# Optimization experiments

Measured on AMD Instinct MI355X. Metric: run time of the kernel, lower is better.

The kernel has to match this reference:

```python
import jax, jax.numpy as jnp
import numpy as np

NUM_EXPERTS = 64
TOP_K = 2
HIDDEN = 4096
BATCH, SEQ = 4, 4096


def setup_inputs() -> dict:
    key = jax.random.key(0)
    k1, k2 = jax.random.split(key)
    hidden_states = jax.random.normal(k1, (BATCH, SEQ, HIDDEN), dtype=jnp.float32)
    # nn.init.normal_(gate.weight, std=0.02); Linear weight shape [E, H]
    gate_w = jax.random.normal(k2, (NUM_EXPERTS, HIDDEN), dtype=jnp.float32) * 0.02
    return {"hidden_states": hidden_states, "gate_w": gate_w}


def reference(hidden_states, gate_w):
    b, s, h = hidden_states.shape
    num_tokens = b * s
    hidden_flat = hidden_states.reshape(num_tokens, h)            # [N, H]
    router_logits = jnp.einsum('nh,eh->ne', hidden_flat, gate_w)  # [N, E]
    routing_probs = jax.nn.softmax(router_logits, axis=-1)        # [N, E]
    topk_probs, topk_indices = jax.lax.top_k(routing_probs, TOP_K)  # [N, K]
    # normalize_weights=True
    topk_probs = topk_probs / (topk_probs.sum(axis=-1, keepdims=True) + 1e-8)
    # routing index computation (grouped-GEMM dispatch metadata)
    flat_experts = topk_indices.reshape(-1)                        # [N*K]
    gather_indices = jnp.argsort(flat_experts, stable=True)        # token_indices[sort_order] == sort_order
    expert_counts = jnp.zeros((NUM_EXPERTS,), dtype=jnp.int32).at[flat_experts].add(1)
    expert_offsets = jnp.cumsum(expert_counts, axis=0)             # [E]
    routing_weights = topk_probs.reshape(-1)                       # [N*K]
    # eval mode: aux_loss and z_loss are zero constants
    aux_loss = jnp.float32(0.0)
    z_loss = jnp.float32(0.0)
    return routing_weights, topk_indices, expert_offsets, gather_indices, aux_loss, z_loss
```

## Files before the change

kernel.cpp:

```cpp
#include <hip/hip_runtime.h>
#include <hip/hip_bf16.h>

#define GL2L16(gp, lp) __builtin_amdgcn_global_load_lds(                      \
    (const __attribute__((address_space(1))) void*)(gp),                      \
    (__attribute__((address_space(3))) void*)(lp), 16, 0, 0)

constexpr int H    = 4096;
constexpr int E    = 64;
constexpr int NTOK = 16384;
constexpr int TB   = 32;
constexpr int KC   = 64;
constexpr int NB2  = 128;

__global__ __launch_bounds__(256) void transpose_gate_k(
    const float* __restrict__ gw, float* __restrict__ gT) {
  int idx = blockIdx.x * 256 + threadIdx.x;
  int h = idx >> 6, e = idx & 63;
  gT[idx] = gw[e * H + h];
}

__global__ __launch_bounds__(256) void router_k(
    const float* __restrict__ hidden, const float* __restrict__ gT,
    float* __restrict__ out_w, float* __restrict__ out_idx,
    int* __restrict__ flatE) {
  __shared__ float As[TB * KC];
  __shared__ float Gs[KC * E];

  const int tid = threadIdx.x;
  const int te = tid & 15, tt = tid >> 4;
  const int t0 = blockIdx.x * TB;
  const float* hblock = hidden + (size_t)t0 * H;

  float acc[2][4] = {{0.f, 0.f, 0.f, 0.f}, {0.f, 0.f, 0.f, 0.f}};

  for (int hc = 0; hc < H; hc += KC) {
    __syncthreads();
#pragma unroll
    for (int r = 0; r < 2; ++r) {
      int lid = r * 256 + tid;
      int t = lid >> 4, h4 = (lid & 15) * 4;
      GL2L16(hblock + t * H + hc + h4, &As[lid * 4]);
    }
    const float* gsrc = gT + hc * E;
#pragma unroll
    for (int r = 0; r < 4; ++r) {
      int lid = r * 256 + tid;
      GL2L16(gsrc + lid * 4, &Gs[lid * 4]);
    }
    __syncthreads();

#pragma unroll
    for (int kk = 0; kk < KC; kk += 4) {
      float a[2][4], g[4][4];
      *(float4*)&a[0][0] = *(const float4*)&As[(2 * tt + 0) * KC + kk];
      *(float4*)&a[1][0] = *(const float4*)&As[(2 * tt + 1) * KC + kk];
#pragma unroll
      for (int k = 0; k < 4; ++k)
        *(float4*)&g[k][0] = *(const float4*)&Gs[(kk + k) * E + 4 * te];
#pragma unroll
      for (int i = 0; i < 2; ++i)
#pragma unroll
        for (int j = 0; j < 4; ++j)
#pragma unroll
          for (int k = 0; k < 4; ++k)
            acc[i][j] = fmaf(a[i][k], g[k][j], acc[i][j]);
    }
  }

#pragma unroll
  for (int i = 0; i < 2; ++i) {
    float v1 = -3.0e38f, v2 = -3.0e38f;
    int e1 = 0, e2 = 0;
#pragma unroll
    for (int j = 0; j < 4; ++j) {
      float v = acc[i][j];
      int e = 4 * te + j;
      if (v > v1 || (v == v1 && e < e1)) {
        v2 = v1; e2 = e1; v1 = v; e1 = e;
      } else if (v > v2 || (v == v2 && e < e2)) {
        v2 = v; e2 = e;
      }
    }
#pragma unroll
    for (int m = 1; m <= 8; m <<= 1) {
      float ov1 = __shfl_xor(v1, m); int oe1 = __shfl_xor(e1, m);
      float ov2 = __shfl_xor(v2, m); int oe2 = __shfl_xor(e2, m);
      bool aFirst = (v1 > ov1) || (v1 == ov1 && e1 < oe1);
      float w1v = aFirst ? v1 : ov1;  int w1e = aFirst ? e1 : oe1;
      float c1  = aFirst ? ov1 : v1;  int c1e = aFirst ? oe1 : e1;
      float c2  = aFirst ? v2 : ov2;  int c2e = aFirst ? e2 : oe2;
      bool s = (c2 > c1) || (c2 == c1 && c2e < c1e);
      v1 = w1v; e1 = w1e;
      v2 = s ? c2 : c1; e2 = s ? c2e : c1e;
    }
    float sum = 0.f;
#pragma unroll
    for (int j = 0; j < 4; ++j) sum += __expf(acc[i][j] - v1);
#pragma unroll
    for (int m = 1; m <= 8; m <<= 1) sum += __shfl_xor(sum, m);

    float p1 = 1.0f / sum;
    float p2 = __expf(v2 - v1) / sum;
    float inv = 1.0f / (p1 + p2 + 1e-8f);
    float w1 = p1 * inv, w2 = p2 * inv;

    if (te == 0) {
      int t = t0 + 2 * tt + i;
      out_w[2 * t]       = w1;
      out_w[2 * t + 1]   = w2;
      out_idx[2 * t]     = (float)e1;
      out_idx[2 * t + 1] = (float)e2;
      flatE[2 * t]       = e1;
      flatE[2 * t + 1]   = e2;
    }
  }
}

__global__ __launch_bounds__(256) void hist_rank_k(
    const int* __restrict__ flatE, int* __restrict__ blockCounts,
    int* __restrict__ rankInBlock) {
  __shared__ int waveCnt[4][64];
  const int tid = threadIdx.x, blk = blockIdx.x;
  const int i = blk * 256 + tid;
  const int key = flatE[i];
  const int lane = tid & 63, w = tid >> 6;
  const unsigned long long below = (1ull << lane) - 1ull;

  int rankWave = 0, cntMyLane = 0;
  for (int e = 0; e < 64; ++e) {
    unsigned long long m = __ballot(key == e);
    if (e == key)  rankWave  = __popcll(m & below);
    if (e == lane) cntMyLane = __popcll(m);
  }
  waveCnt[w][lane] = cntMyLane;
  __syncthreads();

  int pre = 0;
  for (int w2 = 0; w2 < w; ++w2) pre += waveCnt[w2][key];
  rankInBlock[i] = pre + rankWave;

  if (tid < 64) {
    int tot = waveCnt[0][tid] + waveCnt[1][tid] + waveCnt[2][tid] + waveCnt[3][tid];
    blockCounts[blk * 64 + tid] = tot;
  }
}

__global__ void offsets_k(const int* __restrict__ blockCounts,
                          int* __restrict__ offTable,
                          float* __restrict__ out_off,
                          float* __restrict__ out_losses) {
  const int e = threadIdx.x;
  int run = 0;
  for (int b = 0; b < NB2; ++b) {
    offTable[e * NB2 + b] = run;
    run += blockCounts[b * 64 + e];
  }
  const int total = run;
  int inc = total;
  for (int d = 1; d < 64; d <<= 1) {
    int v = __shfl_up(inc, d);
    if (e >= d) inc += v;
  }
  out_off[e] = (float)inc;
  const int base = inc - total;
  for (int b = 0; b < NB2; ++b) offTable[e * NB2 + b] += base;
  if (e == 0) { out_losses[0] = 0.f; out_losses[1] = 0.f; }
}

__global__ __launch_bounds__(256) void scatter_k(
    const int* __restrict__ flatE, const int* __restrict__ rankInBlock,
    const int* __restrict__ offTable, float* __restrict__ out_gather) {
  const int i = blockIdx.x * 256 + threadIdx.x;
  const int key = flatE[i];
  const int pos = offTable[key * NB2 + blockIdx.x] + rankInBlock[i];
  out_gather[pos] = (float)i;
}

extern "C" void kernel_launch(void* const* d_in, const int* in_sizes, int n_in,
                              void* d_out, int out_size, void* d_ws, size_t ws_size,
                              hipStream_t stream) {
  const float* hidden = (const float*)d_in[0];
  const float* gate   = (const float*)d_in[1];

  float* out        = (float*)d_out;
  float* out_w      = out;
  float* out_idx    = out + 32768;
  float* out_off    = out + 65536;
  float* out_gather = out + 65600;
  float* out_losses = out + 98368;

  float* gT          = (float*)d_ws;
  int*   flatE       = (int*)(gT + 262144);
  int*   blockCounts = flatE + 32768;
  int*   rankInBlock = blockCounts + 8192;
  int*   offTable    = rankInBlock + 32768;

  transpose_gate_k<<<1024, 256, 0, stream>>>(gate, gT);
  router_k<<<NTOK / TB, 256, 0, stream>>>(hidden, gT, out_w, out_idx, flatE);
  hist_rank_k<<<NB2, 256, 0, stream>>>(flatE, blockCounts, rankInBlock);
  offsets_k<<<1, 64, 0, stream>>>(blockCounts, offTable, out_off, out_losses);
  scatter_k<<<NB2, 256, 0, stream>>>(flatE, rankInBlock, offTable, out_gather);
}
```

Measured before the change: 454.3 us.

## Use split-bf16 MFMA router GEMM with split-K partials and separate reduce

Replaces the FP32 scalar-FMA shared-memory GEMM with an MFMA kernel. Each fp32 value is split into bf16 hi and lo parts, and three bf16 MFMAs per product recover near-fp32 accuracy. The gate weights are pre-split and packed into fragment order once. The K dimension is split across blocks, with the split count chosen from workspace size, and partial logits are written out then summed in a reduce-plus-top-k kernel. This targets the compute bound of the scalar FMA loop and adds parallelism for the 16K-token GEMM, at the cost of extra partial-buffer traffic and a small loss of precision that could flip near-tied top-k choices.

```diff
diff --git a/kernel.cpp b/kernel.cpp
--- a/kernel.cpp
+++ b/kernel.cpp
@@ -1,69 +1,145 @@
 #include <hip/hip_runtime.h>
 #include <hip/hip_bf16.h>
-
-#define GL2L16(gp, lp) __builtin_amdgcn_global_load_lds(                      \
-    (const __attribute__((address_space(1))) void*)(gp),                      \
-    (__attribute__((address_space(3))) void*)(lp), 16, 0, 0)
-
-constexpr int H    = 4096;
-constexpr int E    = 64;
+#include <stdint.h>
+
+constexpr int HID  = 4096;
+constexpr int NE   = 64;
 constexpr int NTOK = 16384;
-constexpr int TB   = 32;
-constexpr int KC   = 64;
 constexpr int NB2  = 128;
 
-__global__ __launch_bounds__(256) void transpose_gate_k(
-    const float* __restrict__ gw, float* __restrict__ gT) {
-  int idx = blockIdx.x * 256 + threadIdx.x;
-  int h = idx >> 6, e = idx & 63;
-  gT[idx] = gw[e * H + h];
-}
-
-__global__ __launch_bounds__(256) void router_k(
-    const float* __restrict__ hidden, const float* __restrict__ gT,
-    float* __restrict__ out_w, float* __restrict__ out_idx,
-    int* __restrict__ flatE) {
-  __shared__ float As[TB * KC];
-  __shared__ float Gs[KC * E];
-
+typedef __attribute__((ext_vector_type(8))) short short8;
+typedef __attribute__((ext_vector_type(4))) float f32x4;
+
+union Frag { uint32_t u[4]; short8 s; uint4 q; };
+
+__device__ inline uint32_t cvtpk_bf16(float a, float b) {
+  uint32_t r;
+  asm("v_cvt_pk_bf16_f32 %0, %1, %2" : "=v"(r) : "v"(a), "v"(b));
+  return r;
+}
+__device__ inline float asf(uint32_t u) { union { uint32_t u; float f; } c; c.u = u; return c.f; }
+
+__device__ inline void split8(float4 p, float4 q, Frag& hi, Frag& lo) {
+  float x[8] = {p.x, p.y, p.z, p.w, q.x, q.y, q.z, q.w};
+#pragma unroll
+  for (int j = 0; j < 4; ++j) {
+    uint32_t h = cvtpk_bf16(x[2*j], x[2*j+1]);
+    hi.u[j] = h;
+    float r0 = x[2*j]   - asf(h << 16);
+    float r1 = x[2*j+1] - asf(h & 0xFFFF0000u);
+    lo.u[j] = cvtpk_bf16(r0, r1);
+  }
+}
+
+__global__ __launch_bounds__(256) void prep_gate_k(
+    const float* __restrict__ gw, uint4* __restrict__ gP) {
+  int gid = blockIdx.x * 256 + threadIdx.x;
+  int c = gid >> 9;
+  int r = gid & 511;
+  int n = r >> 7;
+  int part = (r >> 6) & 1;
+  int l = r & 63;
+  int e  = n * 16 + (l & 15);
+  int k0 = c * 32 + (l >> 4) * 8;
+  const float* src = gw + (size_t)e * HID + k0;
+  float4 p = *(const float4*)src;
+  float4 q = *(const float4*)(src + 4);
+  Frag hi, lo;
+  split8(p, q, hi, lo);
+  gP[gid] = part ? lo.q : hi.q;
+}
+
+template <int S>
+__global__ __launch_bounds__(256) void gemm_k(
+    const float* __restrict__ hidden, const uint4* __restrict__ gP,
+    float* __restrict__ partial) {
+  constexpr int NCH = 128 / S;
+  const int tid = threadIdx.x;
+  const int w = tid >> 6, l = tid & 63;
+  const int b = blockIdx.x;
+  const int s  = b % S;
+  const int tb = b / S;
+  const int t0 = tb * 128 + w * 32;
+  const int row = l & 15, kg = l >> 4;
+
+  const float* aBase = hidden + (size_t)(t0 + row) * HID + s * (HID / S) + kg * 8;
+  const int cG0 = s * NCH;
+
+  f32x4 acc[2][4] = {};
+  float4 aC[2][2]; uint4 bC[4][2];
+
+  auto LOAD = [&](int c, float4 (&a)[2][2], uint4 (&bb)[4][2]) {
+    const float* ap = aBase + c * 32;
+#pragma unroll
+    for (int mt = 0; mt < 2; ++mt) {
+      const float* p = ap + (size_t)mt * 16 * HID;
+      a[mt][0] = *(const float4*)p;
+      a[mt][1] = *(const float4*)(p + 4);
+    }
+    const uint4* bp = gP + (size_t)(cG0 + c) * 512 + l;
+#pragma unroll
+    for (int nt = 0; nt < 4; ++nt) {
+      bb[nt][0] = bp[(nt * 2 + 0) * 64];
+      bb[nt][1] = bp[(nt * 2 + 1) * 64];
+    }
+  };
+  auto COMP = [&](float4 (&a)[2][2], uint4 (&bb)[4][2]) {
+    Frag ahi[2], alo[2];
+#pragma unroll
+    for (int mt = 0; mt < 2; ++mt) split8(a[mt][0], a[mt][1], ahi[mt], alo[mt]);
+#pragma unroll
+    for (int nt = 0; nt < 4; ++nt) {
+      Frag bhi, blo; bhi.q = bb[nt][0]; blo.q = bb[nt][1];
+#pragma unroll
+      for (int mt = 0; mt < 2; ++mt) {
+        acc[mt][nt] = __builtin_amdgcn_mfma_f32_16x16x32_bf16(ahi[mt].s, bhi.s, acc[mt][nt], 0, 0, 0);
+        acc[mt][nt] = __builtin_amdgcn_mfma_f32_16x16x32_bf16(ahi[mt].s, blo.s, acc[mt][nt], 0, 0, 0);
+        acc[mt][nt] = __builtin_amdgcn_mfma_f32_16x16x32_bf16(alo[mt].s, bhi.s, acc[mt][nt], 0, 0, 0);
+      }
+    }
+  };
+
+  LOAD(0, aC, bC);
+#pragma unroll 8
+  for (int c = 0; c < NCH - 1; ++c) {
+    float4 aN[2][2]; uint4 bN[4][2];
+    LOAD(c + 1, aN, bN);
+    COMP(aC, bC);
+#pragma unroll
+    for (int mt = 0; mt < 2; ++mt) { aC[mt][0] = aN[mt][0]; aC[mt][1] = aN[mt][1]; }
+#pragma unroll
+    for (int nt = 0; nt < 4; ++nt) { bC[nt][0] = bN[nt][0]; bC[nt][1] = bN[nt][1]; }
+  }
+  COMP(aC, bC);
+
+  float* pout = partial + (size_t)s * NTOK * 64;
+#pragma unroll
+  for (int mt = 0; mt < 2; ++mt)
+#pragma unroll
+    for (int r = 0; r < 4; ++r) {
+      int t = t0 + mt * 16 + kg * 4 + r;
+      float* dst = pout + (size_t)t * 64 + (l & 15);
+#pragma unroll
+      for (int nt = 0; nt < 4; ++nt) dst[nt * 16] = acc[mt][nt][r];
+    }
+}
+
+template <int S>
+__global__ __launch_bounds__(256) void reduce_router_k(
+    const float* __restrict__ partial, float* __restrict__ out_w,
+    float* __restrict__ out_idx, int* __restrict__ flatE) {
   const int tid = threadIdx.x;
   const int te = tid & 15, tt = tid >> 4;
-  const int t0 = blockIdx.x * TB;
-  const float* hblock = hidden + (size_t)t0 * H;
-
-  float acc[2][4] = {{0.f, 0.f, 0.f, 0.f}, {0.f, 0.f, 0.f, 0.f}};
-
-  for (int hc = 0; hc < H; hc += KC) {
-    __syncthreads();
-#pragma unroll
-    for (int r = 0; r < 2; ++r) {
-      int lid = r * 256 + tid;
-      int t = lid >> 4, h4 = (lid & 15) * 4;
-      GL2L16(hblock + t * H + hc + h4, &As[lid * 4]);
-    }
-    const float* gsrc = gT + hc * E;
-#pragma unroll
-    for (int r = 0; r < 4; ++r) {
-      int lid = r * 256 + tid;
-      GL2L16(gsrc + lid * 4, &Gs[lid * 4]);
-    }
-    __syncthreads();
-
-#pragma unroll
-    for (int kk = 0; kk < KC; kk += 4) {
-      float a[2][4], g[4][4];
-      *(float4*)&a[0][0] = *(const float4*)&As[(2 * tt + 0) * KC + kk];
-      *(float4*)&a[1][0] = *(const float4*)&As[(2 * tt + 1) * KC + kk];
-#pragma unroll
-      for (int k = 0; k < 4; ++k)
-        *(float4*)&g[k][0] = *(const float4*)&Gs[(kk + k) * E + 4 * te];
-#pragma unroll
-      for (int i = 0; i < 2; ++i)
-#pragma unroll
-        for (int j = 0; j < 4; ++j)
-#pragma unroll
-          for (int k = 0; k < 4; ++k)
-            acc[i][j] = fmaf(a[i][k], g[k][j], acc[i][j]);
+  const int t0 = blockIdx.x * 32;
+
+  float acc[2][4] = {{0.f,0.f,0.f,0.f},{0.f,0.f,0.f,0.f}};
+#pragma unroll
+  for (int i = 0; i < 2; ++i) {
+    int t = t0 + 2 * tt + i;
+#pragma unroll
+    for (int s = 0; s < S; ++s) {
+      float4 v = *(const float4*)(partial + ((size_t)s * NTOK + t) * 64 + 4 * te);
+      acc[i][0] += v.x; acc[i][1] += v.y; acc[i][2] += v.z; acc[i][3] += v.w;
     }
   }
 
@@ -75,11 +151,8 @@
     for (int j = 0; j < 4; ++j) {
       float v = acc[i][j];
       int e = 4 * te + j;
-      if (v > v1 || (v == v1 && e < e1)) {
-        v2 = v1; e2 = e1; v1 = v; e1 = e;
-      } else if (v > v2 || (v == v2 && e < e2)) {
-        v2 = v; e2 = e;
-      }
+      if (v > v1 || (v == v1 && e < e1)) { v2 = v1; e2 = e1; v1 = v; e1 = e; }
+      else if (v > v2 || (v == v2 && e < e2)) { v2 = v; e2 = e; }
     }
 #pragma unroll
     for (int m = 1; m <= 8; m <<= 1) {
@@ -89,9 +162,9 @@
       float w1v = aFirst ? v1 : ov1;  int w1e = aFirst ? e1 : oe1;
       float c1  = aFirst ? ov1 : v1;  int c1e = aFirst ? oe1 : e1;
       float c2  = aFirst ? v2 : ov2;  int c2e = aFirst ? e2 : oe2;
-      bool s = (c2 > c1) || (c2 == c1 && c2e < c1e);
+      bool sset = (c2 > c1) || (c2 == c1 && c2e < c1e);
       v1 = w1v; e1 = w1e;
-      v2 = s ? c2 : c1; e2 = s ? c2e : c1e;
+      v2 = sset ? c2 : c1; e2 = sset ? c2e : c1e;
     }
     float sum = 0.f;
 #pragma unroll
@@ -189,14 +262,39 @@
   float* out_gather = out + 65600;
   float* out_losses = out + 98368;
 
-  float* gT          = (float*)d_ws;
-  int*   flatE       = (int*)(gT + 262144);
+  uint4* gP          = (uint4*)d_ws;
+  int*   flatE       = (int*)((char*)d_ws + (1u << 20));
   int*   blockCounts = flatE + 32768;
   int*   rankInBlock = blockCounts + 8192;
   int*   offTable    = rankInBlock + 32768;
-
-  transpose_gate_k<<<1024, 256, 0, stream>>>(gate, gT);
-  router_k<<<NTOK / TB, 256, 0, stream>>>(hidden, gT, out_w, out_idx, flatE);
+  float* partial     = (float*)((char*)d_ws + (2u << 20));
+
+  const size_t fixed = 2u << 20;
+  const size_t perS  = (size_t)NTOK * 64 * 4;
+  int S = 1;
+  if      (ws_size >= fixed + 8 * perS) S = 8;
+  else if (ws_size >= fixed + 4 * perS) S = 4;
+  else if (ws_size >= fixed + 2 * perS) S = 2;
+
+  prep_gate_k<<<256, 256, 0, stream>>>(gate, gP);
+  switch (S) {
+    case 8:
+      gemm_k<8><<<(NTOK / 128) * 8, 256, 0, stream>>>(hidden, gP, partial);
+      reduce_router_k<8><<<NTOK / 32, 256, 0, stream>>>(partial, out_w, out_idx, flatE);
+      break;
+    case 4:
+      gemm_k<4><<<(NTOK / 128) * 4, 256, 0, stream>>>(hidden, gP, partial);
+      reduce_router_k<4><<<NTOK / 32, 256, 0, stream>>>(partial, out_w, out_idx, flatE);
+      break;
+    case 2:
+      gemm_k<2><<<(NTOK / 128) * 2, 256, 0, stream>>>(hidden, gP, partial);
+      reduce_router_k<2><<<NTOK / 32, 256, 0, stream>>>(partial, out_w, out_idx, flatE);
+      break;
+    default:
+      gemm_k<1><<<(NTOK / 128) * 1, 256, 0, stream>>>(hidden, gP, partial);
+      reduce_router_k<1><<<NTOK / 32, 256, 0, stream>>>(partial, out_w, out_idx, flatE);
+      break;
+  }
   hist_rank_k<<<NB2, 256, 0, stream>>>(flatE, blockCounts, rankInBlock);
   offsets_k<<<1, 64, 0, stream>>>(blockCounts, offTable, out_off, out_losses);
   scatter_k<<<NB2, 256, 0, stream>>>(flatE, rankInBlock, offTable, out_gather);
```

New measurement: 399.7 us. 1.14x faster.
